# Performance work log

Measured on AMD Instinct MI355X. Metric: run time of the kernel, lower is better.

Reference implementation:

```python
import jax, jax.numpy as jnp
import numpy as np

PATCH = 16

def setup_inputs() -> dict:
    key = jax.random.key(0)
    k1, k2 = jax.random.split(key)
    B, C, H, W = 256, 3, 224, 224
    x = jax.random.normal(k1, (B, C, H, W), dtype=jnp.float32)
    # Bernoulli(p=0.5) sample per patch, per batch element: shape (B, W//P, H//P)
    mask = jax.random.randint(k2, (B, W // PATCH, H // PATCH), 0, 2).astype(jnp.bool_)
    return {"x": x, "mask": mask}

def reference(x, mask):
    B, C, H, W = x.shape
    P = PATCH
    h, w = H // P, W // P
    # rearrange 'b c (h p1) (w p2) -> b w h p1 p2 c'
    patches = x.reshape(B, C, h, P, w, P).transpose(0, 4, 2, 3, 5, 1)  # (B, w, h, P, P, C)
    # conditional per-patch transpose 'p1 p2 c -> p2 p1 c' where mask is True
    rotated = jnp.swapaxes(patches, 3, 4)
    patches = jnp.where(mask[:, :, :, None, None, None], rotated, patches)
    # rearrange 'b w h p2 p1 c -> b c (h p2) (w p1)'
    out = patches.transpose(0, 5, 2, 3, 1, 4).reshape(B, C, H, W)
    return out
```

## Files before the change

kernel.cpp:

```cpp
#include <hip/hip_runtime.h>


#define IMG_W 224
#define IMG_HW 50176
#define NPATCH 14

__global__ __launch_bounds__(256) void patch_rotate_kernel(
    const float* __restrict__ x,
    const int*   __restrict__ mask,
    float*       __restrict__ out)
{
    __shared__ float lds[4][16][20];

    const int wv   = threadIdx.x >> 6;
    const int lane = threadIdx.x & 63;
    const int r    = lane >> 2;
    const int q    = lane & 3;

    const int p  = blockIdx.x * 4 + wv;
    const int wi = p % NPATCH;
    int t        = p / NPATCH;
    const int hi = t % NPATCH;
    t            = t / NPATCH;
    const int c  = t % 3;
    const int b  = t / 3;

    const int base = (b * 3 + c) * IMG_HW + hi * (16 * IMG_W) + wi * 16;

    const float4 v = *(const float4*)(x + base + r * IMG_W + 4 * q);

    *(float4*)&lds[wv][r][4 * q] = v;
    __syncthreads();

    const int m = mask[(b * NPATCH + wi) * NPATCH + hi];

    float4 res;
    if (m) {
        res.x = lds[wv][4 * q + 0][r];
        res.y = lds[wv][4 * q + 1][r];
        res.z = lds[wv][4 * q + 2][r];
        res.w = lds[wv][4 * q + 3][r];
    } else {
        res = v;
    }

    *(float4*)(out + base + r * IMG_W + 4 * q) = res;
}

extern "C" void kernel_launch(void* const* d_in, const int* in_sizes, int n_in,
                              void* d_out, int out_size, void* d_ws, size_t ws_size,
                              hipStream_t stream) {
    const float* x    = (const float*)d_in[0];
    const int*   mask = (const int*)d_in[1];
    float*       out  = (float*)d_out;

    const int n_cpatch = in_sizes[0] / 256;
    const int blocks   = n_cpatch / 4;

    patch_rotate_kernel<<<blocks, 256, 0, stream>>>(x, mask, out);
}
```

Baseline: 256.6 us.

## Process full 16-row strips per block with swizzled LDS and persistent grid

Each block now handles a whole 16-row by 224-column strip, so global loads and stores are fully contiguous, replacing the 64-byte row segments touched per patch before. The strip is staged in LDS with an XOR swizzle to avoid bank conflicts on the transposed reads, and the per-strip mask is cached in shared memory. A grid-stride loop with a fixed grid of 1792 blocks replaces one block per four patches. The trade-off is two barriers per strip and hardcoded problem sizes.

After: 266.0 us. 3.7% more time.

```diff
diff --git a/kernel.cpp b/kernel.cpp
--- a/kernel.cpp
+++ b/kernel.cpp
@@ -1,61 +1,69 @@
 #include <hip/hip_runtime.h>
 
 
-#define IMG_W 224
-#define IMG_HW 50176
 #define NPATCH 14
+#define ROWSTRIDE 228
+#define NSTRIPS 10752
+#define F4_PER_STRIP 896
 
 __global__ __launch_bounds__(256) void patch_rotate_kernel(
-    const float* __restrict__ x,
-    const int*   __restrict__ mask,
-    float*       __restrict__ out)
+    const float4* __restrict__ x,
+    const int*    __restrict__ mask,
+    float4*       __restrict__ out)
 {
-    __shared__ float lds[4][16][20];
+    __shared__ float lds[16 * ROWSTRIDE];
+    __shared__ int   smask[NPATCH];
 
-    const int wv   = threadIdx.x >> 6;
-    const int lane = threadIdx.x & 63;
-    const int r    = lane >> 2;
-    const int q    = lane & 3;
+    const int tid = threadIdx.x;
 
-    const int p  = blockIdx.x * 4 + wv;
-    const int wi = p % NPATCH;
-    int t        = p / NPATCH;
-    const int hi = t % NPATCH;
-    t            = t / NPATCH;
-    const int c  = t % 3;
-    const int b  = t / 3;
+    for (int s = blockIdx.x; s < NSTRIPS; s += gridDim.x) {
+        const int hi = s % NPATCH;
+        const int b  = (s / NPATCH) / 3;
 
-    const int base = (b * 3 + c) * IMG_HW + hi * (16 * IMG_W) + wi * 16;
+        if (tid < NPATCH)
+            smask[tid] = mask[(b * NPATCH + tid) * NPATCH + hi];
 
-    const float4 v = *(const float4*)(x + base + r * IMG_W + 4 * q);
+        const float4* __restrict__ src = x + (size_t)s * F4_PER_STRIP;
+        #pragma unroll
+        for (int u = tid; u < F4_PER_STRIP; u += 256) {
+            const float4 v = src[u];
+            const int j  = u / 56;
+            const int G  = u % 56;
+            const int wi = G >> 2, g = G & 3;
+            const int gs = g ^ (j >> 2);
+            *(float4*)&lds[j * ROWSTRIDE + wi * 16 + gs * 4] = v;
+        }
+        __syncthreads();
 
-    *(float4*)&lds[wv][r][4 * q] = v;
-    __syncthreads();
-
-    const int m = mask[(b * NPATCH + wi) * NPATCH + hi];
-
-    float4 res;
-    if (m) {
-        res.x = lds[wv][4 * q + 0][r];
-        res.y = lds[wv][4 * q + 1][r];
-        res.z = lds[wv][4 * q + 2][r];
-        res.w = lds[wv][4 * q + 3][r];
-    } else {
-        res = v;
+        float4* __restrict__ dst = out + (size_t)s * F4_PER_STRIP;
+        #pragma unroll
+        for (int u = tid; u < F4_PER_STRIP; u += 256) {
+            const int i  = u / 56;
+            const int G  = u % 56;
+            const int wi = G >> 2, gl = G & 3;
+            float4 r;
+            if (smask[wi]) {
+                const int colbase = wi * 16 + 4 * ((i >> 2) ^ gl) + (i & 3);
+                r.x = lds[(4 * gl + 0) * ROWSTRIDE + colbase];
+                r.y = lds[(4 * gl + 1) * ROWSTRIDE + colbase];
+                r.z = lds[(4 * gl + 2) * ROWSTRIDE + colbase];
+                r.w = lds[(4 * gl + 3) * ROWSTRIDE + colbase];
+            } else {
+                r = *(const float4*)&lds[i * ROWSTRIDE + wi * 16 +
+                                         4 * (gl ^ (i >> 2))];
+            }
+            dst[u] = r;
+        }
+        __syncthreads();
     }
-
-    *(float4*)(out + base + r * IMG_W + 4 * q) = res;
 }
 
 extern "C" void kernel_launch(void* const* d_in, const int* in_sizes, int n_in,
                               void* d_out, int out_size, void* d_ws, size_t ws_size,
                               hipStream_t stream) {
-    const float* x    = (const float*)d_in[0];
-    const int*   mask = (const int*)d_in[1];
-    float*       out  = (float*)d_out;
+    const float4* x    = (const float4*)d_in[0];
+    const int*    mask = (const int*)d_in[1];
+    float4*       out  = (float4*)d_out;
 
-    const int n_cpatch = in_sizes[0] / 256;
-    const int blocks   = n_cpatch / 4;
-
-    patch_rotate_kernel<<<blocks, 256, 0, stream>>>(x, mask, out);
+    patch_rotate_kernel<<<1792, 256, 0, stream>>>(x, mask, out);
 }
```

## Transpose patches in registers with ds_bpermute, four rows per thread, two iterations per wave

Applied to the files above, without the earlier changes.

Replaces the LDS staging buffer and __syncthreads with cross-lane ds_bpermute shuffles. Each lane now loads a 4x4 sub-tile as four float4 rows, so one wave covers four patches per iteration and loops twice. This removes the block-wide barrier and shared-memory traffic and gives each thread more bytes in flight. In exchange it issues 16 bpermutes per iteration and hardcodes the grid size and image dimensions.

New measurement: 266.5 us. 1.04x slower.

```diff
diff --git a/kernel.cpp b/kernel.cpp
--- a/kernel.cpp
+++ b/kernel.cpp
@@ -1,50 +1,72 @@
 #include <hip/hip_runtime.h>
 
 
-#define IMG_W 224
-#define IMG_HW 50176
 #define NPATCH 14
+
+__device__ __forceinline__ float bperm(int idx, float s) {
+    return __int_as_float(__builtin_amdgcn_ds_bpermute(idx, __float_as_int(s)));
+}
 
 __global__ __launch_bounds__(256) void patch_rotate_kernel(
     const float* __restrict__ x,
     const int*   __restrict__ mask,
     float*       __restrict__ out)
 {
-    __shared__ float lds[4][16][20];
+    const int tid  = threadIdx.x;
+    const int lane = tid & 63;
+    const int wv   = tid >> 6;
+    const int w    = blockIdx.x * 4 + wv;
 
-    const int wv   = threadIdx.x >> 6;
-    const int lane = threadIdx.x & 63;
-    const int r    = lane >> 2;
-    const int q    = lane & 3;
+    const int p  = lane >> 4;
+    const int a  = (lane >> 2) & 3;
+    const int bb = lane & 3;
+    const int lp = (lane & 48) | (bb << 2) | a;
+    const int idx = lp << 2;
 
-    const int p  = blockIdx.x * 4 + wv;
-    const int wi = p % NPATCH;
-    int t        = p / NPATCH;
-    const int hi = t % NPATCH;
-    t            = t / NPATCH;
-    const int c  = t % 3;
-    const int b  = t / 3;
+    #pragma unroll
+    for (int uu = 0; uu < 2; ++uu) {
+        const int u   = 2 * w + uu;
+        const int img = u / 49;
+        const int q   = u % 49;
+        const int n   = 4 * q + p;
+        const int hi  = n / NPATCH;
+        const int wi  = n % NPATCH;
+        const int b   = img / 3;
 
-    const int base = (b * 3 + c) * IMG_HW + hi * (16 * IMG_W) + wi * 16;
+        const int row = hi * 16 + 4 * a;
+        const int col = wi * 16 + 4 * bb;
+        const size_t base = ((size_t)img * 224 + row) * 224 + col;
 
-    const float4 v = *(const float4*)(x + base + r * IMG_W + 4 * q);
+        const float4 v0 = *(const float4*)(x + base);
+        const float4 v1 = *(const float4*)(x + base + 224);
+        const float4 v2 = *(const float4*)(x + base + 448);
+        const float4 v3 = *(const float4*)(x + base + 672);
 
-    *(float4*)&lds[wv][r][4 * q] = v;
-    __syncthreads();
+        const int m = mask[(b * NPATCH + wi) * NPATCH + hi];
 
-    const int m = mask[(b * NPATCH + wi) * NPATCH + hi];
+        float4 B0, B1, B2, B3;
+        B0.x = bperm(idx, v0.x); B0.y = bperm(idx, v0.y);
+        B0.z = bperm(idx, v0.z); B0.w = bperm(idx, v0.w);
+        B1.x = bperm(idx, v1.x); B1.y = bperm(idx, v1.y);
+        B1.z = bperm(idx, v1.z); B1.w = bperm(idx, v1.w);
+        B2.x = bperm(idx, v2.x); B2.y = bperm(idx, v2.y);
+        B2.z = bperm(idx, v2.z); B2.w = bperm(idx, v2.w);
+        B3.x = bperm(idx, v3.x); B3.y = bperm(idx, v3.y);
+        B3.z = bperm(idx, v3.z); B3.w = bperm(idx, v3.w);
 
-    float4 res;
-    if (m) {
-        res.x = lds[wv][4 * q + 0][r];
-        res.y = lds[wv][4 * q + 1][r];
-        res.z = lds[wv][4 * q + 2][r];
-        res.w = lds[wv][4 * q + 3][r];
-    } else {
-        res = v;
+        float4 r0 = v0, r1 = v1, r2 = v2, r3 = v3;
+        if (m) {
+            r0 = make_float4(B0.x, B1.x, B2.x, B3.x);
+            r1 = make_float4(B0.y, B1.y, B2.y, B3.y);
+            r2 = make_float4(B0.z, B1.z, B2.z, B3.z);
+            r3 = make_float4(B0.w, B1.w, B2.w, B3.w);
+        }
+
+        *(float4*)(out + base)       = r0;
+        *(float4*)(out + base + 224) = r1;
+        *(float4*)(out + base + 448) = r2;
+        *(float4*)(out + base + 672) = r3;
     }
-
-    *(float4*)(out + base + r * IMG_W + 4 * q) = res;
 }
 
 extern "C" void kernel_launch(void* const* d_in, const int* in_sizes, int n_in,
@@ -54,8 +76,5 @@
     const int*   mask = (const int*)d_in[1];
     float*       out  = (float*)d_out;
 
-    const int n_cpatch = in_sizes[0] / 256;
-    const int blocks   = n_cpatch / 4;
-
-    patch_rotate_kernel<<<blocks, 256, 0, stream>>>(x, mask, out);
+    patch_rotate_kernel<<<4704, 256, 0, stream>>>(x, mask, out);
 }
```
